# Kernel optimization log

Measured on AMD Instinct MI355X. Metric: run time of the kernel, lower is better.

## Reference

```python
import jax, jax.numpy as jnp
import numpy as np

B, S, D_IN, D_OUT = 4, 2048, 1024, 1024

def setup_inputs() -> dict:
    key = jax.random.key(0)
    k0, k1, k2, k3 = jax.random.split(key, 4)
    sc = 1.0 / np.sqrt(D_IN)
    return {
        "x": jax.random.normal(k0, (B, S, D_IN), dtype=jnp.float32),
        "wq": jax.random.normal(k1, (D_OUT, D_IN), dtype=jnp.float32) * sc,
        "wk": jax.random.normal(k2, (D_OUT, D_IN), dtype=jnp.float32) * sc,
        "wv": jax.random.normal(k3, (D_OUT, D_IN), dtype=jnp.float32) * sc,
    }

def reference(x, wq, wk, wv):
    # Linear (no bias): y = x @ W.T, W shaped [d_out, d_in]
    q = jnp.einsum("bsd,ed->bse", x, wq)
    k = jnp.einsum("bsd,ed->bse", x, wk)
    v = jnp.einsum("bsd,ed->bse", x, wv)
    scores = jnp.einsum("bqe,bke->bqk", q, k)  # [B,S,S]
    n = x.shape[1]
    causal = jnp.triu(jnp.ones((n, n), dtype=bool), k=1)  # True above diagonal -> masked
    scores = jnp.where(causal, -jnp.inf, scores)
    attn = jax.nn.softmax(scores / jnp.sqrt(jnp.asarray(k.shape[-1], scores.dtype)), axis=-1)
    # dropout p=0.0 -> identity
    return jnp.einsum("bqk,bke->bqe", attn, v)
```

## Files before the change

kernel.cpp:

```cpp
#include <hip/hip_runtime.h>

#define Bb 4
#define Ss 2048
#define Dd 1024

typedef unsigned short u16;
typedef __bf16 bf16x8 __attribute__((ext_vector_type(8)));
typedef float  f32x4  __attribute__((ext_vector_type(4)));

__device__ inline u16 f2bf(float f) {
  union { float f; unsigned u; } x; x.f = f;
  unsigned u = x.u;
  return (u16)((u + 0x7fffu + ((u >> 16) & 1u)) >> 16);
}
__device__ inline float bf2f(u16 h) {
  union { unsigned u; float f; } x; x.u = ((unsigned)h) << 16;
  return x.f;
}

__device__ static inline void gl_lds16(const u16* g, u16* l) {
  __builtin_amdgcn_global_load_lds((__attribute__((address_space(1))) const void*)g,
                                   (__attribute__((address_space(3))) void*)l,
                                   16, 0, 0);
}

__device__ static inline void qbar() {
  asm volatile("" ::: "memory");
  __builtin_amdgcn_s_barrier();
  asm volatile("" ::: "memory");
}

template <int GATEN>
__device__ __forceinline__ void qk_gate() {
  if constexpr (GATEN == 7) asm volatile("s_waitcnt vmcnt(7)" ::: "memory");
  else if constexpr (GATEN == 5) asm volatile("s_waitcnt vmcnt(5)" ::: "memory");
  else if constexpr (GATEN == 0) asm volatile("s_waitcnt vmcnt(0)" ::: "memory");
}

__global__ __launch_bounds__(256) void cast_all(const float* __restrict__ x,
                                                const float* __restrict__ wq,
                                                const float* __restrict__ wk,
                                                const float* __restrict__ wv,
                                                u16* __restrict__ xb,
                                                u16* __restrict__ wb,
                                                float* __restrict__ lsum) {
  int id = blockIdx.x;
  if (id < 8) {
    float4 z = {0.f, 0.f, 0.f, 0.f};
    ((float4*)lsum)[id * 256 + threadIdx.x] = z;
  }
  const float* src; u16* dst; int off;
  if (id < 2048) {
    src = x; dst = xb; off = id * 4096;
  } else {
    int wi = id - 2048;
    int w = wi >> 8;
    src = (w == 0) ? wq : (w == 1) ? wk : wv;
    dst = wb + (size_t)w * Dd * Dd;
    off = (wi & 255) * 4096;
  }
#pragma unroll
  for (int t = 0; t < 4; t++) {
    int i = off + t * 1024 + threadIdx.x * 4;
    float4 v = *(const float4*)(src + i);
    unsigned p0 = (unsigned)f2bf(v.x) | ((unsigned)f2bf(v.y) << 16);
    unsigned p1 = (unsigned)f2bf(v.z) | ((unsigned)f2bf(v.w) << 16);
    uint2 p; p.x = p0; p.y = p1;
    *(uint2*)(dst + i) = p;
  }
}

#define BM 128
#define BN 128

__device__ inline void gemm_tile(const u16* __restrict__ A, int lda,
                                 const u16* __restrict__ Bp, int ldb,
                                 int kBeg, int kEnd,
                                 u16* lds, f32x4 acc[4][4]) {
  u16* lA0 = lds;
  u16* lB0 = lds + 4096;
  u16* lA1 = lds + 8192;
  u16* lB1 = lds + 12288;
  const int tid  = threadIdx.x;
  const int lane = tid & 63, wave = tid >> 6;
  const int quad = lane >> 4, r16 = lane & 15;
  const int wm = (wave & 1) * 64, wn = (wave >> 1) * 64;
  const int r0 = tid >> 2, part = tid & 3;

  for (int k0 = kBeg; k0 < kEnd; k0 += 64) {
    __syncthreads();
#pragma unroll
    for (int q = 0; q < 2; q++) {
      int row = q * 64 + r0;
      int s8 = (q * 256 + tid) * 8;
      const u16* ga = A  + (size_t)row * lda + k0 + part * 8;
      const u16* gb = Bp + (size_t)row * ldb + k0 + part * 8;
      gl_lds16(ga,      lA0 + s8);
      gl_lds16(gb,      lB0 + s8);
      gl_lds16(ga + 32, lA1 + s8);
      gl_lds16(gb + 32, lB1 + s8);
    }
    __syncthreads();
#pragma unroll
    for (int h = 0; h < 2; h++) {
      const u16* la = h ? lA1 : lA0;
      const u16* lb = h ? lB1 : lB0;
      bf16x8 fa[4], fb[4];
#pragma unroll
      for (int t = 0; t < 4; t++)
        fa[t] = *(const bf16x8*)(la + (wm + t * 16 + r16) * 32 + quad * 8);
#pragma unroll
      for (int t = 0; t < 4; t++)
        fb[t] = *(const bf16x8*)(lb + (wn + t * 16 + r16) * 32 + quad * 8);
#pragma unroll
      for (int tm = 0; tm < 4; tm++)
#pragma unroll
        for (int tn = 0; tn < 4; tn++)
          acc[tm][tn] = __builtin_amdgcn_mfma_f32_16x16x32_bf16(fa[tm], fb[tn],
                                                                acc[tm][tn], 0, 0, 0);
    }
  }
}

#define QBK 32
#define ABUF 8192
#define BBUF 12288

__global__ __launch_bounds__(512, 1) void qkv_fused(const u16* __restrict__ xb,
                                                    const u16* __restrict__ wb,
                                                    u16* __restrict__ qkv) {
  __shared__ __align__(16) u16 sh[4 * ABUF + 3 * BBUF];

  const int id  = blockIdx.x;
  const int nt  = id & 7, mt = id >> 3;
  const int row0 = mt * 256, col0 = nt * 384;
  const u16* A  = xb + (size_t)row0 * Dd;
  const u16* Bp = wb + (size_t)col0 * Dd;

  const int tid  = threadIdx.x;
  const int lane = tid & 63, wave = tid >> 6;
  const int wr = wave >> 2, wc = wave & 3;
  const int quad = lane >> 4, r16 = lane & 15;

  const int rA0 = tid >> 2,          cA0 = tid & 3;
  const int rA1 = (tid + 512) >> 2,  cA1 = tid & 3;
  const int rB2 = (tid + 1024) >> 2;
  const u16* aS0 = A  + (size_t)rA0 * Dd + (size_t)((cA0 ^ ((rA0 >> 1) & 3)) * 8);
  const u16* aS1 = A  + (size_t)rA1 * Dd + (size_t)((cA1 ^ ((rA1 >> 1) & 3)) * 8);
  const u16* bS0 = Bp + (size_t)rA0 * Dd + (size_t)((cA0 ^ ((rA0 >> 1) & 3)) * 8);
  const u16* bS1 = Bp + (size_t)rA1 * Dd + (size_t)((cA1 ^ ((rA1 >> 1) & 3)) * 8);
  const u16* bS2 = Bp + (size_t)rB2 * Dd + (size_t)((cA0 ^ ((rB2 >> 1) & 3)) * 8);

  auto stgA = [&](int S) {
    u16* d = sh + (S & 3) * ABUF;
    const size_t ko = (size_t)S * QBK;
    gl_lds16(aS0 + ko, d + tid * 8);
    gl_lds16(aS1 + ko, d + (tid + 512) * 8);
  };
  auto stgB = [&](int S) {
    u16* d = sh + 4 * ABUF + ((unsigned)S % 3u) * BBUF;
    const size_t ko = (size_t)S * QBK;
    gl_lds16(bS0 + ko, d + tid * 8);
    gl_lds16(bS1 + ko, d + (tid + 512) * 8);
    gl_lds16(bS2 + ko, d + (tid + 1024) * 8);
  };

  const int chq  = (quad ^ ((r16 >> 1) & 3)) * 8;
  const int idxA = (wr * 128 + r16) * 32 + chq;
  const int idxB = (wc * 96  + r16) * 32 + chq;

  f32x4 acc[8][6];
#pragma unroll
  for (int m = 0; m < 8; m++)
#pragma unroll
    for (int n = 0; n < 6; n++) acc[m][n] = (f32x4){0.f, 0.f, 0.f, 0.f};
  bf16x8 fb[6], fa[4];

#define PH_A(T_, DOB)                                                          \
  {                                                                            \
    const u16* lA = sh + ((T_) & 3) * ABUF;                                    \
    const u16* lB = sh + 4 * ABUF + ((unsigned)(T_) % 3u) * BBUF;              \
    _Pragma("unroll") for (int n = 0; n < 6; n++)                              \
        fb[n] = *(const bf16x8*)(lB + idxB + n * 512);                         \
    _Pragma("unroll") for (int m = 0; m < 4; m++)                              \
        fa[m] = *(const bf16x8*)(lA + idxA + m * 512);                         \
    if (DOB) stgB((T_) + 2);                                                   \
    qbar();                                                                    \
    __builtin_amdgcn_s_setprio(1);                                             \
    _Pragma("unroll") for (int m = 0; m < 4; m++)                              \
      _Pragma("unroll") for (int n = 0; n < 6; n++)                            \
        acc[m][n] = __builtin_amdgcn_mfma_f32_16x16x32_bf16(fa[m], fb[n],      \
                                                            acc[m][n], 0, 0, 0); \
    __builtin_amdgcn_s_setprio(0);                                             \
    qbar();                                                                    \
  }

#define PH_B(T_, DOA, GATEN)                                                   \
  {                                                                            \
    const u16* lA = sh + ((T_) & 3) * ABUF;                                    \
    _Pragma("unroll") for (int m = 0; m < 4; m++)                              \
        fa[m] = *(const bf16x8*)(lA + idxA + (m + 4) * 512);                   \
    if (DOA) stgA((T_) + 3);                                                   \
    qk_gate<GATEN>();                                                          \
    qbar();                                                                    \
    __builtin_amdgcn_s_setprio(1);                                             \
    _Pragma("unroll") for (int m = 0; m < 4; m++)                              \
      _Pragma("unroll") for (int n = 0; n < 6; n++)                            \
        acc[m + 4][n] = __builtin_amdgcn_mfma_f32_16x16x32_bf16(fa[m], fb[n],  \
                                                                acc[m + 4][n], 0, 0, 0); \
    __builtin_amdgcn_s_setprio(0);                                             \
    qbar();                                                                    \
  }

  stgA(0); stgB(0); stgA(1); stgB(1); stgA(2);
  qk_gate<7>();
  qbar();

#pragma unroll 1
  for (int T = 0; T < 29; T++) { PH_A(T, true) PH_B(T, true, 7) }
  PH_A(29, true)  PH_B(29, false, 5)
  PH_A(30, false) PH_B(30, false, 0)
  PH_A(31, false) PH_B(31, false, -1)
#undef PH_A
#undef PH_B

#pragma unroll
  for (int m = 0; m < 8; m++) {
    int rr = row0 + wr * 128 + m * 16 + quad * 4;
#pragma unroll
    for (int n = 0; n < 6; n++) {
      int cc = col0 + wc * 96 + n * 16 + r16;
      u16* o = qkv + (size_t)(cc >> 10) * ((size_t)Bb * Ss * Dd) + (cc & 1023);
#pragma unroll
      for (int r = 0; r < 4; r++)
        o[(size_t)(rr + r) * Dd] = f2bf(acc[m][n][r]);
    }
  }
}

__global__ __launch_bounds__(256) void scores_fused(const u16* __restrict__ qb,
                                                    const u16* __restrict__ kb,
                                                    const u16* __restrict__ vb,
                                                    u16* __restrict__ sc,
                                                    u16* __restrict__ vt,
                                                    float* __restrict__ lsum) {
  __shared__ __align__(16) u16 shmem[16384];
  const int id = blockIdx.x;
  const int tid = threadIdx.x;

  if (id >= 544) {
    const int bid = id - 544;
    u16 (*t)[72] = (u16(*)[72])shmem;
    for (int u = bid; u < 2048; u += 480) {
      const int b = u >> 9, rem = u & 511;
      const int e0 = (rem >> 5) * 64, s0 = (rem & 31) * 64;
      const u16* src = vb + (size_t)b * Ss * Dd;
      u16* dst = vt + (size_t)b * Dd * Ss;
      if (u != bid) __syncthreads();
#pragma unroll
      for (int gg = tid; gg < 512; gg += 256) {
        int row = gg >> 3, prt = gg & 7;
        uint4 v = *(const uint4*)(src + (size_t)(s0 + row) * Dd + e0 + prt * 8);
        const u16* pv = (const u16*)&v;
#pragma unroll
        for (int jj = 0; jj < 8; jj++) t[prt * 8 + jj][row] = pv[jj];
      }
      __syncthreads();
#pragma unroll
      for (int gg = tid; gg < 512; gg += 256) {
        int ee = gg >> 3, prt = gg & 7;
        uint4 v = *(const uint4*)(&t[ee][prt * 8]);
        *(uint4*)(dst + (size_t)(e0 + ee) * Ss + s0 + prt * 8) = v;
      }
    }
    return;
  }

  const int xcd = id & 7, j = id >> 3;
  const int b = j / 17, tloc = j - b * 17;
  const int t = xcd * 17 + tloc;
  int it = (int)((sqrtf(8.f * (float)t + 1.f) - 1.f) * 0.5f);
  while ((it + 1) * (it + 2) / 2 <= t) it++;
  while (it * (it + 1) / 2 > t) it--;
  const int jt = t - it * (it + 1) / 2;

  const u16* A  = qb + (size_t)b * Ss * Dd + (size_t)it * BM * Dd;
  const u16* Bp = kb + (size_t)b * Ss * Dd + (size_t)jt * BN * Dd;
  f32x4 acc[4][4];
  const f32x4 zero = {0.f, 0.f, 0.f, 0.f};
#pragma unroll
  for (int tm = 0; tm < 4; tm++)
#pragma unroll
    for (int tn = 0; tn < 4; tn++) acc[tm][tn] = zero;

  gemm_tile(A, Dd, Bp, Dd, 0, Dd, shmem, acc);

  u16* out = sc + (size_t)b * Ss * Ss;
  float* lr = lsum + (size_t)b * Ss;
  const int lane = tid & 63, wave = tid >> 6;
  const int quad = lane >> 4, r16 = lane & 15;
  const int wm = (wave & 1) * 64, wn = (wave >> 1) * 64;
#pragma unroll
  for (int tm = 0; tm < 4; tm++) {
    float psum[4] = {0.f, 0.f, 0.f, 0.f};
#pragma unroll
    for (int tn = 0; tn < 4; tn++) {
      int rr = it * BM + wm + tm * 16 + quad * 4;
      int cc = jt * BN + wn + tn * 16 + r16;
#pragma unroll
      for (int r = 0; r < 4; r++) {
        float p = 0.f;
        u16 h = 0;
        if (cc <= rr + r) {
          h = f2bf(__expf(acc[tm][tn][r] * 0.03125f));
          p = bf2f(h);
        }
        out[(size_t)(rr + r) * Ss + cc] = h;
        psum[r] += p;
      }
    }
#pragma unroll
    for (int r = 0; r < 4; r++) {
      float s = psum[r];
      s += __shfl_xor(s, 1);
      s += __shfl_xor(s, 2);
      s += __shfl_xor(s, 4);
      s += __shfl_xor(s, 8);
      if (r16 == 0) {
        int row = it * BM + wm + tm * 16 + quad * 4 + r;
        atomicAdd(&lr[row], s);
      }
    }
  }
}

__global__ __launch_bounds__(256) void pv_gemm(const u16* __restrict__ sc,
                                               const u16* __restrict__ vt,
                                               const float* __restrict__ lsum,
                                               float* __restrict__ out) {
  __shared__ __align__(16) u16 shmem[16384];
  const int idx = blockIdx.x;
  const int xcd = idx & 7, slot = idx >> 3;
  const int qp = slot >> 3, col = slot & 7;
  const int b = qp & 3;
  const int it = (qp >> 2) ? (15 - xcd) : xcd;
  const int row0 = it * BM;
  const int col0 = col * BN;
  const u16* A  = sc + (size_t)b * Ss * Ss + (size_t)row0 * Ss;
  const u16* Bp = vt + (size_t)b * Dd * Ss + (size_t)col0 * Ss;
  f32x4 acc[4][4];
  const f32x4 zero = {0.f, 0.f, 0.f, 0.f};
#pragma unroll
  for (int tm = 0; tm < 4; tm++)
#pragma unroll
    for (int tn = 0; tn < 4; tn++) acc[tm][tn] = zero;

  gemm_tile(A, Ss, Bp, Ss, 0, row0 + BM, shmem, acc);

  float* o = out + (size_t)b * Ss * Dd;
  const float* lr = lsum + (size_t)b * Ss;
  const int lane = threadIdx.x & 63, wave = threadIdx.x >> 6;
  const int quad = lane >> 4, r16 = lane & 15;
  const int wm = (wave & 1) * 64, wn = (wave >> 1) * 64;
#pragma unroll
  for (int tm = 0; tm < 4; tm++) {
    int rbase = row0 + wm + tm * 16 + quad * 4;
    float s0 = 1.f / lr[rbase], s1 = 1.f / lr[rbase + 1];
    float s2 = 1.f / lr[rbase + 2], s3 = 1.f / lr[rbase + 3];
#pragma unroll
    for (int tn = 0; tn < 4; tn++) {
      int cc = col0 + wn + tn * 16 + r16;
      o[(size_t)(rbase + 0) * Dd + cc] = acc[tm][tn][0] * s0;
      o[(size_t)(rbase + 1) * Dd + cc] = acc[tm][tn][1] * s1;
      o[(size_t)(rbase + 2) * Dd + cc] = acc[tm][tn][2] * s2;
      o[(size_t)(rbase + 3) * Dd + cc] = acc[tm][tn][3] * s3;
    }
  }
}

extern "C" void kernel_launch(void* const* d_in, const int* in_sizes, int n_in,
                              void* d_out, int out_size, void* d_ws, size_t ws_size,
                              hipStream_t stream) {
  const float* x  = (const float*)d_in[0];
  const float* wq = (const float*)d_in[1];
  const float* wk = (const float*)d_in[2];
  const float* wv = (const float*)d_in[3];
  float* out = (float*)d_out;
  char* ws = (char*)d_ws;
  if (ws_size < 106987520u) return;

  u16* qkv  = (u16*)(ws);
  u16* sc   = (u16*)(ws + 50331648u);
  u16* xb   = (u16*)(ws + 83886080u);
  u16* vt   = xb;
  u16* wb   = (u16*)(ws + 100663296u);
  float* lsum = (float*)(ws + 106954752u);

  const size_t nQ = (size_t)Bb * Ss * Dd;

  cast_all<<<2816, 256, 0, stream>>>(x, wq, wk, wv, xb, wb, lsum);
  qkv_fused<<<256, 512, 0, stream>>>(xb, wb, qkv);
  scores_fused<<<1024, 256, 0, stream>>>(qkv, qkv + nQ, qkv + 2 * nQ, sc, vt, lsum);
  pv_gemm<<<512, 256, 0, stream>>>(sc, vt, lsum, out);
}
```

Before: 242.2 us.

## Restructure QKV GEMM main loop into four sub-phases with A-fragment prefetch

```diff
diff --git a/kernel.cpp b/kernel.cpp
--- a/kernel.cpp
+++ b/kernel.cpp
@@ -126,9 +126,11 @@
 #define ABUF 8192
 #define BBUF 12288
 
-__global__ __launch_bounds__(512, 1) void qkv_fused(const u16* __restrict__ xb,
-                                                    const u16* __restrict__ wb,
-                                                    u16* __restrict__ qkv) {
+__global__ __launch_bounds__(512)
+__attribute__((amdgpu_waves_per_eu(2)))
+void qkv_fused(const u16* __restrict__ xb,
+               const u16* __restrict__ wb,
+               u16* __restrict__ qkv) {
   __shared__ __align__(16) u16 sh[4 * ABUF + 3 * BBUF];
 
   const int id  = blockIdx.x;
@@ -174,40 +176,54 @@
   for (int m = 0; m < 8; m++)
 #pragma unroll
     for (int n = 0; n < 6; n++) acc[m][n] = (f32x4){0.f, 0.f, 0.f, 0.f};
-  bf16x8 fb[6], fa[4];
-
-#define PH_A(T_, DOB)                                                          \
+  bf16x8 faA[4], faB[4], fbL[3], fbH[3];
+
+#define REGION(T_, DO_B, DO_A, GATEN, DO_PF)                                   \
   {                                                                            \
     const u16* lA = sh + ((T_) & 3) * ABUF;                                    \
     const u16* lB = sh + 4 * ABUF + ((unsigned)(T_) % 3u) * BBUF;              \
-    _Pragma("unroll") for (int n = 0; n < 6; n++)                              \
-        fb[n] = *(const bf16x8*)(lB + idxB + n * 512);                         \
-    _Pragma("unroll") for (int m = 0; m < 4; m++)                              \
-        fa[m] = *(const bf16x8*)(lA + idxA + m * 512);                         \
-    if (DOB) stgB((T_) + 2);                                                   \
-    qbar();                                                                    \
+                                                                       \
+    _Pragma("unroll") for (int n = 0; n < 3; n++)                              \
+        fbL[n] = *(const bf16x8*)(lB + idxB + n * 512);                        \
+    _Pragma("unroll") for (int n = 0; n < 3; n++)                              \
+        fbH[n] = *(const bf16x8*)(lB + idxB + (n + 3) * 512);                  \
     __builtin_amdgcn_s_setprio(1);                                             \
     _Pragma("unroll") for (int m = 0; m < 4; m++)                              \
-      _Pragma("unroll") for (int n = 0; n < 6; n++)                            \
-        acc[m][n] = __builtin_amdgcn_mfma_f32_16x16x32_bf16(fa[m], fb[n],      \
+      _Pragma("unroll") for (int n = 0; n < 3; n++)                            \
+        acc[m][n] = __builtin_amdgcn_mfma_f32_16x16x32_bf16(faA[m], fbL[n],    \
                                                             acc[m][n], 0, 0, 0); \
     __builtin_amdgcn_s_setprio(0);                                             \
-    qbar();                                                                    \
-  }
-
-#define PH_B(T_, DOA, GATEN)                                                   \
-  {                                                                            \
-    const u16* lA = sh + ((T_) & 3) * ABUF;                                    \
+                                                                       \
     _Pragma("unroll") for (int m = 0; m < 4; m++)                              \
-        fa[m] = *(const bf16x8*)(lA + idxA + (m + 4) * 512);                   \
-    if (DOA) stgA((T_) + 3);                                                   \
+        faB[m] = *(const bf16x8*)(lA + idxA + (m + 4) * 512);                  \
+    if (DO_B) stgB((T_) + 2);                                                  \
+    __builtin_amdgcn_s_setprio(1);                                             \
+    _Pragma("unroll") for (int m = 0; m < 4; m++)                              \
+      _Pragma("unroll") for (int n = 0; n < 3; n++)                            \
+        acc[m][n + 3] = __builtin_amdgcn_mfma_f32_16x16x32_bf16(faA[m], fbH[n], \
+                                                            acc[m][n + 3], 0, 0, 0); \
+    __builtin_amdgcn_s_setprio(0);                                             \
+                                                                       \
+    if (DO_A) stgA((T_) + 3);                                                  \
     qk_gate<GATEN>();                                                          \
     qbar();                                                                    \
+    if (DO_PF) {                                                               \
+      const u16* lA1_ = sh + (((T_) + 1) & 3) * ABUF;                          \
+      _Pragma("unroll") for (int m = 0; m < 4; m++)                            \
+          faA[m] = *(const bf16x8*)(lA1_ + idxA + m * 512);                    \
+    }                                                                          \
     __builtin_amdgcn_s_setprio(1);                                             \
     _Pragma("unroll") for (int m = 0; m < 4; m++)                              \
-      _Pragma("unroll") for (int n = 0; n < 6; n++)                            \
-        acc[m + 4][n] = __builtin_amdgcn_mfma_f32_16x16x32_bf16(fa[m], fb[n],  \
-                                                                acc[m + 4][n], 0, 0, 0); \
+      _Pragma("unroll") for (int n = 0; n < 3; n++)                            \
+        acc[m + 4][n] = __builtin_amdgcn_mfma_f32_16x16x32_bf16(faB[m], fbL[n], \
+                                                            acc[m + 4][n], 0, 0, 0); \
+    __builtin_amdgcn_s_setprio(0);                                             \
+                                                                       \
+    __builtin_amdgcn_s_setprio(1);                                             \
+    _Pragma("unroll") for (int m = 0; m < 4; m++)                              \
+      _Pragma("unroll") for (int n = 0; n < 3; n++)                            \
+        acc[m + 4][n + 3] = __builtin_amdgcn_mfma_f32_16x16x32_bf16(faB[m], fbH[n], \
+                                                            acc[m + 4][n + 3], 0, 0, 0); \
     __builtin_amdgcn_s_setprio(0);                                             \
     qbar();                                                                    \
   }
@@ -215,14 +231,16 @@
   stgA(0); stgB(0); stgA(1); stgB(1); stgA(2);
   qk_gate<7>();
   qbar();
+#pragma unroll
+  for (int m = 0; m < 4; m++)
+    faA[m] = *(const bf16x8*)(sh + idxA + m * 512);
 
 #pragma unroll 1
-  for (int T = 0; T < 29; T++) { PH_A(T, true) PH_B(T, true, 7) }
-  PH_A(29, true)  PH_B(29, false, 5)
-  PH_A(30, false) PH_B(30, false, 0)
-  PH_A(31, false) PH_B(31, false, -1)
-#undef PH_A
-#undef PH_B
+  for (int T = 0; T < 29; T++) REGION(T, true, true, 7, true);
+  REGION(29, true,  false, 5, true)
+  REGION(30, false, false, 0, true)
+  REGION(31, false, false, -1, false)
+#undef REGION
 
 #pragma unroll
   for (int m = 0; m < 8; m++) {
```

After: 267.0 us. 1.1x slower.
